# Performance work log

Measured on AMD Instinct MI355X. Metric: run time of the kernel, lower is better.

Reference implementation:

```python
import jax, jax.numpy as jnp
import numpy as np

H, W = 1080, 1920
NPART = 25          # BODY_25 joint parts (channel 25 is background)
NLIMB = 26          # 26 PAF limbs -> 52 PAF channels
K = 32              # max peaks kept per joint (static top-k)
MID = 10            # mid_num line samples
THRE1 = 0.1
SIGMA = 3.0
RADIUS = 12         # scipy gaussian_filter: int(truncate*sigma+0.5), truncate=4
# BODY_25 limb sequence (SKEL25DEF.paf_dict), paired with mapIdx [[2k,2k+1]]
LIMBS = np.array([[1,8],[1,2],[1,5],[2,3],[3,4],[5,6],[6,7],[8,9],[9,10],
                  [10,11],[8,12],[12,13],[13,14],[1,0],[0,15],[15,16],[0,17],
                  [0,18],[14,19],[19,20],[14,21],[11,22],[22,23],[11,24],
                  [2,17],[5,18]], dtype=np.int32)


def gaussian_blur(x):
    """Separable gaussian filter, sigma=3, scipy mode='reflect' (= np symmetric). x: [H,W,C]."""
    C = x.shape[-1]
    t = jnp.arange(-RADIUS, RADIUS + 1, dtype=x.dtype)
    k = jnp.exp(-0.5 * (t / SIGMA) ** 2)
    k = k / k.sum()
    dn = ('NHWC', 'HWIO', 'NHWC')
    # vertical pass
    xp = jnp.pad(x, ((RADIUS, RADIUS), (0, 0), (0, 0)), mode='symmetric')[None]
    kh = jnp.tile(k.reshape(-1, 1, 1, 1), (1, 1, 1, C))
    x1 = jax.lax.conv_general_dilated(xp, kh, (1, 1), 'VALID',
                                      dimension_numbers=dn, feature_group_count=C)
    # horizontal pass
    x1 = jnp.pad(x1, ((0, 0), (0, 0), (RADIUS, RADIUS), (0, 0)), mode='symmetric')
    kw = jnp.tile(k.reshape(1, -1, 1, 1), (1, 1, 1, C))
    x2 = jax.lax.conv_general_dilated(x1, kw, (1, 1), 'VALID',
                                      dimension_numbers=dn, feature_group_count=C)
    return x2[0]


def openpose_post(heatmap_avg, paf_avg):
    maps = heatmap_avg[:, :, :NPART]                      # [H,W,25] map_ori per part
    sm = gaussian_blur(maps)                              # one_heatmap per part
    z_row = jnp.zeros((1, W, NPART), sm.dtype)
    z_col = jnp.zeros((H, 1, NPART), sm.dtype)
    m_left = jnp.concatenate([z_row, sm[:-1]], axis=0)
    m_right = jnp.concatenate([sm[1:], z_row], axis=0)
    m_up = jnp.concatenate([z_col, sm[:, :-1]], axis=1)
    m_down = jnp.concatenate([sm[:, 1:], z_col], axis=1)
    peaks_bin = ((sm >= m_left) & (sm >= m_right) & (sm >= m_up)
                 & (sm >= m_down) & (sm > THRE1))
    # static per-part top-K peaks, scored by the ORIGINAL (unblurred) map value
    flat = jnp.where(peaks_bin, maps, -1e9).transpose(2, 0, 1).reshape(NPART, H * W)
    vals, idx = jax.lax.top_k(flat, K)                    # [25,K]
    mask = vals > -1e8
    py = (idx // W).astype(jnp.int32)
    px = (idx % W).astype(jnp.int32)
    peak_x = px.astype(maps.dtype)
    peak_y = py.astype(maps.dtype)
    peak_scores = jnp.where(mask, vals, 0.0)

    limbs = jnp.asarray(LIMBS)
    ax, ay, ma = peak_x[limbs[:, 0]], peak_y[limbs[:, 0]], mask[limbs[:, 0]]  # [26,K]
    bx, by, mb = peak_x[limbs[:, 1]], peak_y[limbs[:, 1]], mask[limbs[:, 1]]
    paf_pairs = jnp.moveaxis(paf_avg.reshape(H, W, NLIMB, 2), 2, 0)           # [26,H,W,2]

    def limb_conn(paf2, ax, ay, bx, by, ma, mb):
        vx = bx[None, :] - ax[:, None]                    # [K,K]
        vy = by[None, :] - ay[:, None]
        norm = jnp.sqrt(vx * vx + vy * vy) + 1e-10
        ux, uy = vx / norm, vy / norm
        t = jnp.linspace(0.0, 1.0, MID, dtype=ax.dtype)   # matches np.linspace(a,b,10)
        sx = jnp.round(ax[:, None, None] + vx[:, :, None] * t).astype(jnp.int32)  # [K,K,MID]
        sy = jnp.round(ay[:, None, None] + vy[:, :, None] * t).astype(jnp.int32)
        pvx = paf2[sy, sx, 0]
        pvy = paf2[sy, sx, 1]
        score = (pvx * ux[:, :, None] + pvy * uy[:, :, None]).mean(-1)
        score = jnp.clip(score, 0.0, 1.0)
        return jnp.where(ma[:, None] & mb[None, :], score, 0.0)

    conn = jax.vmap(limb_conn)(paf_pairs, ax, ay, bx, by, ma, mb)             # [26,K,K]
    return peak_x, peak_y, peak_scores, mask, conn


def setup_inputs() -> dict:
    key = jax.random.key(0)
    k1, k2 = jax.random.split(key)
    heatmap_avg = jax.random.uniform(k1, (H, W, NPART + 1), dtype=jnp.float32)
    paf_avg = jax.random.normal(k2, (H, W, 2 * NLIMB), dtype=jnp.float32) * 0.3
    return {"heatmap_avg": heatmap_avg, "paf_avg": paf_avg}


def reference(heatmap_avg, paf_avg):
    return openpose_post(heatmap_avg, paf_avg)
```

## Files before the change

kernel.cpp:

```cpp
#include <hip/hip_runtime.h>
#include <math.h>
#include <float.h>

#define H 1080
#define W 1920
#define HWSZ (H*W)
#define NPART 25
#define NCH 26
#define NLIMB 26
#define KTOP 32
#define MID 10
#define RAD 12

#define EPS1 4e-6f
#define EPS2 1.5e-7
#define BLCAP (1 << 20)
#define NS 16

#define VB 10
#define VXT 16
#define VCHUNK 100
#define TH2S 30
#define TW2B 256
#define VTC2 282
#define VTS2 283
#define SMS2 257
#define CANDC 2048

#define OFF_PY   800
#define OFF_SC   1600
#define OFF_MK   2400
#define OFF_CONN 3200

__device__ __constant__ int LIMBS_d[NLIMB * 2] = {
    1,8, 1,2, 1,5, 2,3, 3,4, 5,6, 6,7, 8,9, 9,10, 10,11, 8,12, 12,13, 13,14,
    1,0, 0,15, 15,16, 0,17, 0,18, 14,19, 19,20, 14,21, 11,22, 22,23, 11,24, 2,17, 5,18
};

__device__ __forceinline__ int symH(int y) {
    if (y < 0) return -1 - y;
    if (y >= H) return 2 * H - 1 - y;
    return y;
}
__device__ __forceinline__ int symW(int x) {
    if (x < 0) return -1 - x;
    if (x >= W) return 2 * W - 1 - x;
    return x;
}

__global__ void winit_k(double* __restrict__ gw64, float* __restrict__ gw32)
{
    if (threadIdx.x == 0) {
        double wd[25]; double s = 0.0;
        for (int t = 0; t < 25; ++t) {
            double u = (double)(t - 12) / 3.0;
            wd[t] = exp(-0.5 * u * u); s += wd[t];
        }
        for (int t = 0; t < 13; ++t) {
            double w = wd[t] / s;
            gw64[t] = w;
            gw32[t] = (float)w;
        }
    }
}

__global__ __launch_bounds__(416) void vert_k(
    const float* __restrict__ hm, float* __restrict__ vpl,
    const double* __restrict__ gw64)
{
    __shared__ float ldv[VB][26][17];
    const int tid = threadIdx.x;
    const int x0 = blockIdx.x * VXT;
    const int ys = blockIdx.y * VCHUNK;
    const int c  = tid % 26;
    const int xo = tid / 26;
    const int gx = x0 + xo;

    double ws[13];
    #pragma unroll
    for (int t = 0; t < 13; ++t) ws[t] = gw64[t];

    const size_t cstr = (size_t)W * NCH;
    const size_t base = (size_t)gx * NCH + c;
    const bool yint = (ys >= 12) && (ys + VCHUNK + 11 < H);

    double win[25];
    if (yint) {
        const float* p0 = hm + (size_t)(ys - 12) * cstr + base;
        #pragma unroll
        for (int k = 0; k < 24; ++k) { win[k] = (double)*p0; p0 += cstr; }
    } else {
        #pragma unroll
        for (int k = 0; k < 24; ++k) {
            int ry = symH(ys - 12 + k);
            win[k] = (double)hm[(size_t)ry * cstr + base];
        }
    }
    win[24] = 0.0;

    const float* pn = hm + (size_t)symH(ys + 12) * cstr + base;

    #pragma unroll 1
    for (int blk = 0; blk < VCHUNK; blk += 25) {
        #pragma unroll
        for (int p = 0; p < 25; ++p) {
            const int yo = blk + p;
            const int y  = ys + yo;
            double nv;
            if (yint) { nv = (double)*pn; pn += cstr; }
            else      { int ry = symH(y + 12); nv = (double)hm[(size_t)ry * cstr + base]; }
            win[(p + 24) % 25] = nv;
            double acc = 0.0;
            #pragma unroll
            for (int t = 0; t < 25; ++t)
                acc = fma(ws[t < 13 ? t : 24 - t], win[(p + t) % 25], acc);
            if (c < 25) ldv[yo % VB][c][xo] = (float)acc;
            if ((yo % VB) == VB - 1) {
                __syncthreads();
                const int c2 = tid >> 4, x2 = tid & 15;
                if (c2 < 25) {
                    const int yb = ys + yo - (VB - 1);
                    #pragma unroll
                    for (int i = 0; i < VB; ++i) {
                        int yr = yb + i;
                        if (yr < H)
                            vpl[(size_t)c2 * HWSZ + (size_t)yr * W + x0 + x2] = ldv[i][c2][x2];
                    }
                }
                __syncthreads();
            }
        }
    }
}

__global__ __launch_bounds__(512) void horiz_nms_k(
    const float* __restrict__ vpl, const float* __restrict__ hm,
    float* __restrict__ cval, int* __restrict__ cidx,
    int* __restrict__ counters, unsigned int* __restrict__ blg,
    const float* __restrict__ gw32, int cap)
{
    __shared__ __align__(16) float ubuf[32 * VTS2];
    float (*vt)[VTS2]  = reinterpret_cast<float(*)[VTS2]>(ubuf);
    float (*smt)[SMS2] = reinterpret_cast<float(*)[SMS2]>(ubuf);
    __shared__ unsigned short cand[CANDC];
    __shared__ unsigned int bl[1024];
    __shared__ int lcount, bcount, gbase, gbase2;

    const int tid = threadIdx.x;
    const int r   = tid & 31;
    const int g   = tid >> 5;
    const int ch  = blockIdx.z;
    const int x0  = blockIdx.x * TW2B;
    const int y0  = blockIdx.y * TH2S;
    const float* vp = vpl + (size_t)ch * HWSZ;

    if (tid == 0) { lcount = 0; bcount = 0; }
    float w32[13];
    #pragma unroll
    for (int t = 0; t < 13; ++t) w32[t] = gw32[t];

    {
        const int lr  = tid >> 4;
        const int lc0 = tid & 15;
        int gy = y0 - 1 + lr;
        gy = gy < 0 ? 0 : (gy >= H ? H - 1 : gy);
        const float* rowp = vp + (size_t)gy * W;
        const bool xint = (x0 >= 13) && (x0 + (VTC2 - 13) <= W);
        if (xint) {
            const float* p = rowp + (x0 - 13) + lc0;
            #pragma unroll
            for (int j = 0; j < 18; ++j) {
                int cc = lc0 + 16 * j;
                if (cc < VTC2) vt[lr][cc] = p[16 * j];
            }
        } else {
            #pragma unroll
            for (int j = 0; j < 18; ++j) {
                int cc = lc0 + 16 * j;
                if (cc < VTC2) vt[lr][cc] = rowp[symW(x0 - 13 + cc)];
            }
        }
    }
    __syncthreads();

    float a[18];
    #pragma unroll
    for (int k = 0; k < 18; ++k) a[k] = 0.f;
    {
        const float* vrow = &vt[r][g * 16];
        #pragma unroll
        for (int t = 0; t < 42; ++t) {
            float x = vrow[t];
            #pragma unroll
            for (int k = 0; k < 18; ++k)
                if (t >= k && t < k + 25) {
                    int wi = t - k; wi = wi < 13 ? wi : 24 - wi;
                    a[k] = fmaf(w32[wi], x, a[k]);
                }
        }
    }
    __syncthreads();

    const int gy_r = y0 - 1 + r;
    {
        const bool rowok = (gy_r >= 0 && gy_r < H);
        #pragma unroll
        for (int k = 1; k <= 16; ++k) {
            int j = g * 16 + k - 1;
            int gxj = x0 + j;
            smt[r][j] = (rowok && gxj < W) ? a[k] : 0.f;
        }
    }
    __syncthreads();

    if (r >= 1 && r <= TH2S && gy_r < H) {
        const float* up = &smt[r - 1][g * 16];
        const float* dn = &smt[r + 1][g * 16];
        const int ly = r - 1;
        #pragma unroll
        for (int k = 0; k < 16; ++k) {
            int gx = x0 + g * 16 + k;
            if (gx >= W) continue;
            float s  = a[k + 1];
            float lv = (gx == 0) ? 0.f : a[k];
            float rv = (gx + 1 >= W) ? 0.f : a[k + 2];
            float dT = s - 0.1f;
            float d0 = s - up[k];
            float d1 = s - dn[k];
            float d2 = s - lv;
            float d3 = s - rv;
            int flags = (fabsf(dT) <= EPS1 ? 1 : 0)
                      | (fabsf(d0) <= EPS1 ? 2 : 0)
                      | (fabsf(d1) <= EPS1 ? 4 : 0)
                      | (fabsf(d2) <= EPS1 ? 8 : 0)
                      | (fabsf(d3) <= EPS1 ? 16 : 0);
            if (!flags) {
                if (dT > 0.f && d0 >= 0.f && d1 >= 0.f && d2 >= 0.f && d3 >= 0.f) {
                    int pos = atomicAdd(&lcount, 1);
                    int gpix = (y0 + ly) * W + gx;
                    if (pos < CANDC) cand[pos] = (unsigned short)((ly << 8) | (g * 16 + k));
                    else {
                        int p = atomicAdd(&counters[ch], 1);
                        if (p < cap) {
                            cval[(size_t)ch * cap + p] = hm[(size_t)gpix * NCH + ch];
                            cidx[(size_t)ch * cap + p] = gpix;
                        }
                    }
                }
            } else {
                bool fail = (!(flags & 1)  && dT <= 0.f) ||
                            (!(flags & 2)  && d0 <  0.f) ||
                            (!(flags & 4)  && d1 <  0.f) ||
                            (!(flags & 8)  && d2 <  0.f) ||
                            (!(flags & 16) && d3 <  0.f);
                if (!fail) {
                    unsigned int ent = ((unsigned int)ch << 26) | ((unsigned int)flags << 21)
                                     | (unsigned int)((y0 + ly) * W + gx);
                    int bp = atomicAdd(&bcount, 1);
                    if (bp < 1024) bl[bp] = ent;
                    else {
                        int gp = atomicAdd(&counters[32], 1);
                        if (gp < BLCAP) blg[gp] = ent;
                    }
                }
            }
        }
    }
    __syncthreads();

    if (tid == 0) {
        int nl = lcount < CANDC ? lcount : CANDC;
        gbase  = atomicAdd(&counters[ch], nl);
        int nb = bcount < 1024 ? bcount : 1024;
        gbase2 = atomicAdd(&counters[32], nb);
    }
    __syncthreads();
    int n = lcount < CANDC ? lcount : CANDC;
    int b = gbase;
    for (int i = tid; i < n; i += 512) {
        int p = b + i;
        if (p < cap) {
            int e = cand[i];
            int ly = e >> 8, lx = e & 255;
            int gpix = (y0 + ly) * W + (x0 + lx);
            cval[(size_t)ch * cap + p] = hm[(size_t)gpix * NCH + ch];
            cidx[(size_t)ch * cap + p] = gpix;
        }
    }
    int nb = bcount < 1024 ? bcount : 1024;
    for (int i = tid; i < nb; i += 512) {
        int gp = gbase2 + i;
        if (gp < BLCAP) blg[gp] = bl[i];
    }
}

__device__ __forceinline__ double smh2(const float* __restrict__ vp,
                                       const double* w64s, int y, int x)
{
    int lane = threadIdx.x & 63;
    double term = 0.0;
    if (lane < 25) {
        int cx = symW(x - RAD + lane);
        int wi = lane < 13 ? lane : 24 - lane;
        term = w64s[wi] * (double)vp[(size_t)y * W + cx];
    }
    #pragma unroll
    for (int off = 16; off > 0; off >>= 1)
        term += __shfl_xor(term, off, 64);
    return __shfl(term, 0, 64);
}

__device__ double sm64_eval(const float* __restrict__ hm, int ch,
                            const double* w64s, int y, int x)
{
    int lane = threadIdx.x & 63;
    double colsum = 0.0;
    if (lane < 25) {
        int cx = symW(x - RAD + lane);
        float xv[25];
        #pragma unroll
        for (int t = 0; t < 25; t++) {
            int ry = symH(y - RAD + t);
            xv[t] = hm[((size_t)ry * W + cx) * NCH + ch];
        }
        #pragma unroll
        for (int t = 0; t < 25; t++)
            colsum = fma(w64s[t < 13 ? t : 24 - t], (double)xv[t], colsum);
    }
    double acc = 0.0;
    for (int ci = 0; ci < 25; ci++) {
        double cs = __shfl(colsum, ci, 64);
        acc = fma(w64s[ci < 13 ? ci : 24 - ci], cs, acc);
    }
    return acc;
}

__global__ __launch_bounds__(64) void recheck_k(
    const float* __restrict__ vpl, const float* __restrict__ hm,
    float* __restrict__ cval, int* __restrict__ cidx,
    int* __restrict__ counters, const unsigned int* __restrict__ blg,
    const double* __restrict__ gw64, int cap)
{
    __shared__ double w64s[13];
    const int tid = threadIdx.x;
    if (tid < 13) w64s[tid] = gw64[tid];
    __syncthreads();

    int total = counters[32];
    if (total > BLCAP) total = BLCAP;
    for (int e = blockIdx.x; e < total; e += gridDim.x) {
        unsigned int ent = blg[e];
        int ch    = (int)(ent >> 26);
        int flags = (int)((ent >> 21) & 31);
        int gpix  = (int)(ent & 0x1FFFFFu);
        int gy = gpix / W, gx = gpix - gy * W;
        const float* vp = vpl + (size_t)ch * HWSZ;

        double sc = smh2(vp, w64s, gy, gx);
        bool dead = false; bool esc = false;
        if (flags & 1) {
            double d = sc - 0.1;
            if (d <= -EPS2) dead = true; else if (d < EPS2) esc = true;
        }
        if (!dead && (flags & 2)) {
            double nv = (gy - 1 >= 0) ? smh2(vp, w64s, gy - 1, gx) : 0.0;
            double d = sc - nv;
            if (d <= -EPS2) dead = true; else if (d < EPS2) esc = true;
        }
        if (!dead && (flags & 4)) {
            double nv = (gy + 1 < H) ? smh2(vp, w64s, gy + 1, gx) : 0.0;
            double d = sc - nv;
            if (d <= -EPS2) dead = true; else if (d < EPS2) esc = true;
        }
        if (!dead && (flags & 8)) {
            double nv = (gx - 1 >= 0) ? smh2(vp, w64s, gy, gx - 1) : 0.0;
            double d = sc - nv;
            if (d <= -EPS2) dead = true; else if (d < EPS2) esc = true;
        }
        if (!dead && (flags & 16)) {
            double nv = (gx + 1 < W) ? smh2(vp, w64s, gy, gx + 1) : 0.0;
            double d = sc - nv;
            if (d <= -EPS2) dead = true; else if (d < EPS2) esc = true;
        }
        bool accept = false;
        if (!dead && !esc) accept = true;
        else if (!dead && esc) {
            double sE = sm64_eval(hm, ch, w64s, gy, gx);
            bool ok = (flags & 1) ? (sE > 0.1) : true;
            if (ok && (flags & 2))  { double nv = (gy - 1 >= 0) ? sm64_eval(hm, ch, w64s, gy - 1, gx) : 0.0; ok = (sE >= nv); }
            if (ok && (flags & 4))  { double nv = (gy + 1 <  H) ? sm64_eval(hm, ch, w64s, gy + 1, gx) : 0.0; ok = (sE >= nv); }
            if (ok && (flags & 8))  { double nv = (gx - 1 >= 0) ? sm64_eval(hm, ch, w64s, gy, gx - 1) : 0.0; ok = (sE >= nv); }
            if (ok && (flags & 16)) { double nv = (gx + 1 <  W) ? sm64_eval(hm, ch, w64s, gy, gx + 1) : 0.0; ok = (sE >= nv); }
            accept = ok;
        }
        if (accept && tid == 0) {
            int p = atomicAdd(&counters[ch], 1);
            if (p < cap) {
                cval[(size_t)ch * cap + p] = hm[(size_t)gpix * NCH + ch];
                cidx[(size_t)ch * cap + p] = gpix;
            }
        }
    }
}

#define TH 32
#define TW 64
#define LR (TH + 2*RAD + 2)
#define LC 90
#define VRR 34
#define VC (TW + 2*RAD + 2)
#define SR 34
#define SC 66
__global__ __launch_bounds__(256) void blur_peaks_gather(
    const float* __restrict__ hm,
    float* __restrict__ cval, int* __restrict__ cidx,
    int* __restrict__ counters, int cap)
{
    __shared__ float  in_t[LR][LC];
    __shared__ double v[VRR][VC];
    __shared__ double smv[SR][SC];
    __shared__ double wgt[2 * RAD + 1];
    __shared__ double wsum;

    const int tid = threadIdx.x;
    const int ch  = blockIdx.x;
    const int x0  = blockIdx.y * TW;
    const int y0  = blockIdx.z * TH;

    if (tid < 2 * RAD + 1) {
        double t = (double)(tid - RAD) / 3.0;
        wgt[tid] = exp(-0.5 * t * t);
    }
    __syncthreads();
    if (tid == 0) {
        double s = 0.0;
        for (int i = 0; i < 2 * RAD + 1; i++) s += wgt[i];
        wsum = s;
    }
    __syncthreads();
    if (tid < 2 * RAD + 1) wgt[tid] /= wsum;

    for (int i = tid; i < LR * LC; i += 256) {
        int r = i / LC, c = i % LC;
        int gy = symH(y0 - RAD - 1 + r);
        int gx = symW(x0 - RAD - 1 + c);
        in_t[r][c] = hm[((size_t)gy * W + gx) * NCH + ch];
    }
    __syncthreads();

    for (int i = tid; i < VRR * VC; i += 256) {
        int r = i / VC, c = i % VC;
        double acc = 0.0;
        #pragma unroll
        for (int t = 0; t < 2 * RAD + 1; t++)
            acc = fma(wgt[t], (double)in_t[r + t][c], acc);
        v[r][c] = acc;
    }
    __syncthreads();

    for (int i = tid; i < SR * SC; i += 256) {
        int r = i / SC, cc = i % SC;
        int gy = y0 - 1 + r;
        int gx = x0 - 1 + cc;
        double acc = 0.0;
        if (gy >= 0 && gy < H && gx >= 0 && gx < W) {
            #pragma unroll
            for (int t = 0; t < 2 * RAD + 1; t++)
                acc = fma(wgt[t], v[r][cc + t], acc);
        }
        smv[r][cc] = acc;
    }
    __syncthreads();

    for (int i = tid; i < TH * TW; i += 256) {
        int ly = i / TW, lx = i % TW;
        int gy = y0 + ly, gx = x0 + lx;
        if (gy >= H || gx >= W) continue;
        double s = smv[ly + 1][lx + 1];
        if (s > 0.1 &&
            s >= smv[ly][lx + 1] && s >= smv[ly + 2][lx + 1] &&
            s >= smv[ly + 1][lx] && s >= smv[ly + 1][lx + 2]) {
            float val = in_t[ly + RAD + 1][lx + RAD + 1];
            int pos = atomicAdd(&counters[ch], 1);
            if (pos < cap) {
                cval[(size_t)ch * cap + pos] = val;
                cidx[(size_t)ch * cap + pos] = gy * W + gx;
            }
        }
    }
}

#define BT 128
__global__ __launch_bounds__(BT) void topk1_kernel(
    const float* __restrict__ cval, const int* __restrict__ cidx,
    const int* __restrict__ counters, int cap,
    unsigned long long* __restrict__ s1)
{
    __shared__ unsigned long long lk[KTOP * BT];
    __shared__ unsigned long long rk[BT];
    __shared__ int rw[BT];
    __shared__ int winner;

    const int tid = threadIdx.x;
    const int sl  = blockIdx.x;
    const int ch  = blockIdx.y;
    int n = counters[ch];
    if (n > cap) n = cap;

    int cnt = 0;
    for (int j = sl * BT + tid; j < n; j += NS * BT) {
        float v = cval[(size_t)ch * cap + j];
        unsigned int u = __float_as_uint(v);
        u = (u & 0x80000000u) ? ~u : (u | 0x80000000u);
        unsigned long long key =
            ((unsigned long long)u << 32) |
            (unsigned int)(0xFFFFFFFFu - (unsigned int)cidx[(size_t)ch * cap + j]);
        if (cnt == KTOP) {
            if (key <= lk[(KTOP - 1) * BT + tid]) continue;
            cnt = KTOP - 1;
        }
        int i = cnt;
        while (i > 0 && key > lk[(i - 1) * BT + tid]) {
            lk[i * BT + tid] = lk[(i - 1) * BT + tid];
            i--;
        }
        lk[i * BT + tid] = key;
        cnt++;
    }
    int cur = 0;
    __syncthreads();

    for (int k = 0; k < KTOP; k++) {
        rk[tid] = (cur < cnt) ? lk[cur * BT + tid] : 0ULL;
        rw[tid] = tid;
        __syncthreads();
        for (int s = BT / 2; s > 0; s >>= 1) {
            if (tid < s) {
                if (rk[tid + s] > rk[tid]) { rk[tid] = rk[tid + s]; rw[tid] = rw[tid + s]; }
            }
            __syncthreads();
        }
        if (tid == 0) {
            winner = rw[0];
            s1[((size_t)ch * NS + sl) * KTOP + k] = rk[0];
        }
        __syncthreads();
        if (tid == winner && cur < cnt) cur++;
        __syncthreads();
    }
}

__global__ __launch_bounds__(BT) void topk2_kernel(
    const unsigned long long* __restrict__ s1,
    const int* __restrict__ counters, int cap, float* __restrict__ out)
{
    __shared__ unsigned long long sk[NS * KTOP];
    const int tid = threadIdx.x;
    const int ch  = blockIdx.x;

    for (int i = tid; i < NS * KTOP; i += BT)
        sk[i] = s1[(size_t)ch * NS * KTOP + i];
    __syncthreads();

    for (int k = 2; k <= NS * KTOP; k <<= 1) {
        for (int j = k >> 1; j > 0; j >>= 1) {
            for (int t = tid; t < NS * KTOP; t += BT) {
                int ixj = t ^ j;
                if (ixj > t) {
                    unsigned long long a = sk[t], b = sk[ixj];
                    bool sw = ((t & k) == 0) ? (a < b) : (a > b);
                    if (sw) { sk[t] = b; sk[ixj] = a; }
                }
            }
            __syncthreads();
        }
    }

    int n = counters[ch];
    if (n > cap) n = cap;
    if (tid < KTOP) {
        unsigned long long bk = sk[tid];
        float px, py, sc, mk;
        if (bk == 0ULL) {
            int fake = tid - n; if (fake < 0) fake = 0;
            px = (float)(fake % W); py = (float)(fake / W); sc = 0.f; mk = 0.f;
        } else {
            unsigned int u = (unsigned int)(bk >> 32);
            unsigned int fb = (u & 0x80000000u) ? (u ^ 0x80000000u) : ~u;
            float v = __uint_as_float(fb);
            int idx = (int)(0xFFFFFFFFu - (unsigned int)(bk & 0xFFFFFFFFu));
            px = (float)(idx % W); py = (float)(idx / W); sc = v; mk = 1.f;
        }
        out[ch * KTOP + tid]          = px;
        out[OFF_PY + ch * KTOP + tid] = py;
        out[OFF_SC + ch * KTOP + tid] = sc;
        out[OFF_MK + ch * KTOP + tid] = mk;
    }
}

__global__ __launch_bounds__(BT) void topk_kernel(
    const float* __restrict__ cval, const int* __restrict__ cidx,
    const int* __restrict__ counters, int cap, float* __restrict__ out)
{
    __shared__ unsigned long long lk[KTOP * BT];
    __shared__ unsigned long long rk[BT];
    __shared__ int rw[BT];
    __shared__ int winner;

    const int tid = threadIdx.x;
    const int ch  = blockIdx.x;
    int n = counters[ch];
    if (n > cap) n = cap;

    int cnt = 0;
    for (int j = tid; j < n; j += BT) {
        float v = cval[(size_t)ch * cap + j];
        unsigned int u = __float_as_uint(v);
        u = (u & 0x80000000u) ? ~u : (u | 0x80000000u);
        unsigned long long key =
            ((unsigned long long)u << 32) |
            (unsigned int)(0xFFFFFFFFu - (unsigned int)cidx[(size_t)ch * cap + j]);
        if (cnt == KTOP) {
            if (key <= lk[(KTOP - 1) * BT + tid]) continue;
            cnt = KTOP - 1;
        }
        int i = cnt;
        while (i > 0 && key > lk[(i - 1) * BT + tid]) {
            lk[i * BT + tid] = lk[(i - 1) * BT + tid];
            i--;
        }
        lk[i * BT + tid] = key;
        cnt++;
    }
    int cur = 0;
    __syncthreads();

    for (int k = 0; k < KTOP; k++) {
        rk[tid] = (cur < cnt) ? lk[cur * BT + tid] : 0ULL;
        rw[tid] = tid;
        __syncthreads();
        for (int s = BT / 2; s > 0; s >>= 1) {
            if (tid < s) {
                if (rk[tid + s] > rk[tid]) { rk[tid] = rk[tid + s]; rw[tid] = rw[tid + s]; }
            }
            __syncthreads();
        }
        if (tid == 0) {
            winner = rw[0];
            unsigned long long bk = rk[0];
            float px, py, sc, mk;
            if (bk == 0ULL) {
                int fake = k - n; if (fake < 0) fake = 0;
                px = (float)(fake % W); py = (float)(fake / W); sc = 0.f; mk = 0.f;
            } else {
                unsigned int u = (unsigned int)(bk >> 32);
                unsigned int fb = (u & 0x80000000u) ? (u ^ 0x80000000u) : ~u;
                float v = __uint_as_float(fb);
                int idx = (int)(0xFFFFFFFFu - (unsigned int)(bk & 0xFFFFFFFFu));
                px = (float)(idx % W); py = (float)(idx / W); sc = v; mk = 1.f;
            }
            out[ch * KTOP + k]          = px;
            out[OFF_PY + ch * KTOP + k] = py;
            out[OFF_SC + ch * KTOP + k] = sc;
            out[OFF_MK + ch * KTOP + k] = mk;
        }
        __syncthreads();
        if (tid == winner && cur < cnt) cur++;
        __syncthreads();
    }
}

__global__ __launch_bounds__(1024) void limbs_kernel(
    const float* __restrict__ pk, const float* __restrict__ paf,
    float* __restrict__ out)
{
    const int l = blockIdx.x;
    const int tid = threadIdx.x;
    const int i = tid >> 5;
    const int j = tid & 31;
    const int A = LIMBS_d[2 * l], B = LIMBS_d[2 * l + 1];

    float ax = pk[A * KTOP + i],          ay = pk[OFF_PY + A * KTOP + i];
    float ma = pk[OFF_MK + A * KTOP + i];
    float bx = pk[B * KTOP + j],          by = pk[OFF_PY + B * KTOP + j];
    float mb = pk[OFF_MK + B * KTOP + j];

    float vx = bx - ax, vy = by - ay;
    float norm = sqrtf(vx * vx + vy * vy) + 1e-10f;
    float ux = vx / norm, uy = vy / norm;

    const float step = 1.0f / 9.0f;
    float sum = 0.f;
    #pragma unroll
    for (int m = 0; m < MID; m++) {
        float t = (float)m * step;
        int sx = (int)rintf(ax + vx * t);
        int sy = (int)rintf(ay + vy * t);
        const float* p = paf + ((size_t)sy * W + sx) * (2 * NLIMB) + 2 * l;
        sum += p[0] * ux + p[1] * uy;
    }
    float score = sum / (float)MID;
    score = score < 0.f ? 0.f : (score > 1.f ? 1.f : score);
    float res = (ma != 0.f && mb != 0.f) ? score : 0.f;
    out[OFF_CONN + l * (KTOP * KTOP) + i * KTOP + j] = res;
}

extern "C" void kernel_launch(void* const* d_in, const int* in_sizes, int n_in,
                              void* d_out, int out_size, void* d_ws, size_t ws_size,
                              hipStream_t stream)
{
    const float* hm  = (const float*)d_in[0];
    const float* paf = (const float*)d_in[1];
    float* out = (float*)d_out;

    const size_t vpl_bytes = (size_t)NPART * HWSZ * sizeof(float);
    const size_t bl_bytes  = (size_t)BLCAP * 4;
    const size_t s1_bytes  = (size_t)NPART * NS * KTOP * 8;
    const size_t head = 512;

    bool pathA = false;
    int cap = 1;
    if (ws_size > head + vpl_bytes + bl_bytes + s1_bytes
                 + (size_t)NPART * 8 * 4096 + 1024) {
        size_t avail = ws_size - head - vpl_bytes - bl_bytes - s1_bytes - 1024;
        long long c = (long long)(avail / ((size_t)NPART * 8));
        cap = c > 65536 ? 65536 : (int)c;
        pathA = true;
    } else {
        size_t avail = ws_size > head ? ws_size - head : 0;
        long long c = (long long)(avail / ((size_t)NPART * 8));
        cap = c > 65536 ? 65536 : (int)c;
        if (cap < 1) cap = 1;
    }

    int*    counters = (int*)d_ws;
    double* gw64 = (double*)((char*)d_ws + 256);
    float*  gw32 = (float*)((char*)d_ws + 384);
    float* cval = (float*)((char*)d_ws + head);
    int*   cidx = (int*)(cval + (size_t)NPART * cap);
    unsigned long long* s1 = (unsigned long long*)(cidx + (size_t)NPART * cap);
    unsigned int* blg = (unsigned int*)(s1 + (pathA ? (size_t)NPART * NS * KTOP : 0));
    float* vpl = (float*)(blg + (pathA ? (size_t)BLCAP : 0));
    vpl = (float*)(((uintptr_t)vpl + 255) & ~(uintptr_t)255);

    hipMemsetAsync(d_ws, 0, 256, stream);

    if (pathA) {
        winit_k<<<1, 64, 0, stream>>>(gw64, gw32);
        dim3 g1(W / VXT, (H + VCHUNK - 1) / VCHUNK);
        vert_k<<<g1, 416, 0, stream>>>(hm, vpl, gw64);
        dim3 g2((W + TW2B - 1) / TW2B, H / TH2S, NPART);
        horiz_nms_k<<<g2, 512, 0, stream>>>(vpl, hm, cval, cidx, counters, blg, gw32, cap);
        recheck_k<<<2048, 64, 0, stream>>>(vpl, hm, cval, cidx, counters, blg, gw64, cap);
        dim3 gt(NS, NPART);
        topk1_kernel<<<gt, BT, 0, stream>>>(cval, cidx, counters, cap, s1);
        topk2_kernel<<<NPART, BT, 0, stream>>>(s1, counters, cap, out);
    } else {
        dim3 gA(NPART, (W + TW - 1) / TW, (H + TH - 1) / TH);
        blur_peaks_gather<<<gA, 256, 0, stream>>>(hm, cval, cidx, counters, cap);
        topk_kernel<<<NPART, BT, 0, stream>>>(cval, cidx, counters, cap, out);
    }
    limbs_kernel<<<NLIMB, 1024, 0, stream>>>(out, paf, out);
}
```

Before: 442.3 us.

## Fuse double-precision borderline recheck into horizontal NMS kernel using LDS tile

Borderline peak candidates are now rechecked in double precision inside horiz_nms_k, reading the vertical-pass tile already held in shared memory. This replaces the global borderline list and the separate wave-per-entry recheck kernel that re-read vpl. Only the rare ambiguous cases are escalated to a smaller exact-evaluation kernel. Up/down neighbour values now come from wave shuffles instead of a second shared-memory pass with two barriers, and vert_k skips loads for the idle 26th channel lane. The cost is more divergent double-precision work inside the NMS kernel and a smaller global escalation buffer capacity.

```diff
diff --git a/kernel.cpp b/kernel.cpp
--- a/kernel.cpp
+++ b/kernel.cpp
@@ -14,7 +14,7 @@
 
 #define EPS1 4e-6f
 #define EPS2 1.5e-7
-#define BLCAP (1 << 20)
+#define B3CAP 65536
 #define NS 16
 
 #define VB 10
@@ -24,8 +24,7 @@
 #define TW2B 256
 #define VTC2 282
 #define VTS2 283
-#define SMS2 257
-#define CANDC 2048
+#define CANDC 1024
 
 #define OFF_PY   800
 #define OFF_SC   1600
@@ -75,6 +74,7 @@
     const int c  = tid % 26;
     const int xo = tid / 26;
     const int gx = x0 + xo;
+    const bool act = (c < 25);
 
     double ws[13];
     #pragma unroll
@@ -85,18 +85,21 @@
     const bool yint = (ys >= 12) && (ys + VCHUNK + 11 < H);
 
     double win[25];
-    if (yint) {
-        const float* p0 = hm + (size_t)(ys - 12) * cstr + base;
-        #pragma unroll
-        for (int k = 0; k < 24; ++k) { win[k] = (double)*p0; p0 += cstr; }
-    } else {
-        #pragma unroll
-        for (int k = 0; k < 24; ++k) {
-            int ry = symH(ys - 12 + k);
-            win[k] = (double)hm[(size_t)ry * cstr + base];
-        }
-    }
-    win[24] = 0.0;
+    #pragma unroll
+    for (int k = 0; k < 25; ++k) win[k] = 0.0;
+    if (act) {
+        if (yint) {
+            const float* p0 = hm + (size_t)(ys - 12) * cstr + base;
+            #pragma unroll
+            for (int k = 0; k < 24; ++k) { win[k] = (double)*p0; p0 += cstr; }
+        } else {
+            #pragma unroll
+            for (int k = 0; k < 24; ++k) {
+                int ry = symH(ys - 12 + k);
+                win[k] = (double)hm[(size_t)ry * cstr + base];
+            }
+        }
+    }
 
     const float* pn = hm + (size_t)symH(ys + 12) * cstr + base;
 
@@ -106,15 +109,15 @@
         for (int p = 0; p < 25; ++p) {
             const int yo = blk + p;
             const int y  = ys + yo;
-            double nv;
-            if (yint) { nv = (double)*pn; pn += cstr; }
-            else      { int ry = symH(y + 12); nv = (double)hm[(size_t)ry * cstr + base]; }
+            double nv = 0.0;
+            if (yint) { if (act) nv = (double)*pn; pn += cstr; }
+            else if (act) { int ry = symH(y + 12); nv = (double)hm[(size_t)ry * cstr + base]; }
             win[(p + 24) % 25] = nv;
             double acc = 0.0;
             #pragma unroll
             for (int t = 0; t < 25; ++t)
                 acc = fma(ws[t < 13 ? t : 24 - t], win[(p + t) % 25], acc);
-            if (c < 25) ldv[yo % VB][c][xo] = (float)acc;
+            if (act) ldv[yo % VB][c][xo] = (float)acc;
             if ((yo % VB) == VB - 1) {
                 __syncthreads();
                 const int c2 = tid >> 4, x2 = tid & 15;
@@ -133,18 +136,28 @@
     }
 }
 
+__device__ __forceinline__ double smh2_lds(const float (*vt)[VTS2],
+                                           const double* __restrict__ gw64,
+                                           int row, int cb)
+{
+    double acc = 0.0;
+    #pragma unroll
+    for (int t = 0; t < 25; ++t) {
+        int wi = t < 13 ? t : 24 - t;
+        acc = fma(gw64[wi], (double)vt[row][cb + t], acc);
+    }
+    return acc;
+}
+
 __global__ __launch_bounds__(512) void horiz_nms_k(
     const float* __restrict__ vpl, const float* __restrict__ hm,
     float* __restrict__ cval, int* __restrict__ cidx,
-    int* __restrict__ counters, unsigned int* __restrict__ blg,
-    const float* __restrict__ gw32, int cap)
-{
-    __shared__ __align__(16) float ubuf[32 * VTS2];
-    float (*vt)[VTS2]  = reinterpret_cast<float(*)[VTS2]>(ubuf);
-    float (*smt)[SMS2] = reinterpret_cast<float(*)[SMS2]>(ubuf);
+    int* __restrict__ counters, unsigned int* __restrict__ bl3,
+    const float* __restrict__ gw32, const double* __restrict__ gw64, int cap)
+{
+    __shared__ __align__(16) float vt[32][VTS2];
     __shared__ unsigned short cand[CANDC];
-    __shared__ unsigned int bl[1024];
-    __shared__ int lcount, bcount, gbase, gbase2;
+    __shared__ int lcount, gbase;
 
     const int tid = threadIdx.x;
     const int r   = tid & 31;
@@ -154,7 +167,7 @@
     const int y0  = blockIdx.y * TH2S;
     const float* vp = vpl + (size_t)ch * HWSZ;
 
-    if (tid == 0) { lcount = 0; bcount = 0; }
+    if (tid == 0) lcount = 0;
     float w32[13];
     #pragma unroll
     for (int t = 0; t < 13; ++t) w32[t] = gw32[t];
@@ -199,23 +212,16 @@
                 }
         }
     }
-    __syncthreads();
-
-    const int gy_r = y0 - 1 + r;
-    {
-        const bool rowok = (gy_r >= 0 && gy_r < H);
-        #pragma unroll
-        for (int k = 1; k <= 16; ++k) {
-            int j = g * 16 + k - 1;
-            int gxj = x0 + j;
-            smt[r][j] = (rowok && gxj < W) ? a[k] : 0.f;
-        }
-    }
-    __syncthreads();
-
-    if (r >= 1 && r <= TH2S && gy_r < H) {
-        const float* up = &smt[r - 1][g * 16];
-        const float* dn = &smt[r + 1][g * 16];
+
+    float upv[16], dnv[16];
+    #pragma unroll
+    for (int k = 0; k < 16; ++k) {
+        upv[k] = __shfl_up(a[k + 1], 1, 64);
+        dnv[k] = __shfl_down(a[k + 1], 1, 64);
+    }
+
+    const int gy = y0 - 1 + r;
+    if (r >= 1 && r <= TH2S && gy < H) {
         const int ly = r - 1;
         #pragma unroll
         for (int k = 0; k < 16; ++k) {
@@ -224,9 +230,11 @@
             float s  = a[k + 1];
             float lv = (gx == 0) ? 0.f : a[k];
             float rv = (gx + 1 >= W) ? 0.f : a[k + 2];
+            float u0 = (gy - 1 >= 0) ? upv[k] : 0.f;
+            float d0v = (gy + 1 < H) ? dnv[k] : 0.f;
             float dT = s - 0.1f;
-            float d0 = s - up[k];
-            float d1 = s - dn[k];
+            float d0 = s - u0;
+            float d1 = s - d0v;
             float d2 = s - lv;
             float d3 = s - rv;
             int flags = (fabsf(dT) <= EPS1 ? 1 : 0)
@@ -234,19 +242,10 @@
                       | (fabsf(d1) <= EPS1 ? 4 : 0)
                       | (fabsf(d2) <= EPS1 ? 8 : 0)
                       | (fabsf(d3) <= EPS1 ? 16 : 0);
+            bool emit = false;
+            bool esc  = false;
             if (!flags) {
-                if (dT > 0.f && d0 >= 0.f && d1 >= 0.f && d2 >= 0.f && d3 >= 0.f) {
-                    int pos = atomicAdd(&lcount, 1);
-                    int gpix = (y0 + ly) * W + gx;
-                    if (pos < CANDC) cand[pos] = (unsigned short)((ly << 8) | (g * 16 + k));
-                    else {
-                        int p = atomicAdd(&counters[ch], 1);
-                        if (p < cap) {
-                            cval[(size_t)ch * cap + p] = hm[(size_t)gpix * NCH + ch];
-                            cidx[(size_t)ch * cap + p] = gpix;
-                        }
-                    }
-                }
+                emit = (dT > 0.f && d0 >= 0.f && d1 >= 0.f && d2 >= 0.f && d3 >= 0.f);
             } else {
                 bool fail = (!(flags & 1)  && dT <= 0.f) ||
                             (!(flags & 2)  && d0 <  0.f) ||
@@ -254,25 +253,63 @@
                             (!(flags & 8)  && d2 <  0.f) ||
                             (!(flags & 16) && d3 <  0.f);
                 if (!fail) {
-                    unsigned int ent = ((unsigned int)ch << 26) | ((unsigned int)flags << 21)
-                                     | (unsigned int)((y0 + ly) * W + gx);
-                    int bp = atomicAdd(&bcount, 1);
-                    if (bp < 1024) bl[bp] = ent;
-                    else {
-                        int gp = atomicAdd(&counters[32], 1);
-                        if (gp < BLCAP) blg[gp] = ent;
+                    const int cb = g * 16 + k + 1;
+                    double s2 = smh2_lds(vt, gw64, r, cb);
+                    bool dead = false;
+                    if (flags & 1) {
+                        double d = s2 - 0.1;
+                        if (d <= -EPS2) dead = true; else if (d < EPS2) esc = true;
+                    }
+                    if (!dead && (flags & 2)) {
+                        double nv = (gy - 1 >= 0) ? smh2_lds(vt, gw64, r - 1, cb) : 0.0;
+                        double d = s2 - nv;
+                        if (d <= -EPS2) dead = true; else if (d < EPS2) esc = true;
+                    }
+                    if (!dead && (flags & 4)) {
+                        double nv = (gy + 1 < H) ? smh2_lds(vt, gw64, r + 1, cb) : 0.0;
+                        double d = s2 - nv;
+                        if (d <= -EPS2) dead = true; else if (d < EPS2) esc = true;
+                    }
+                    if (!dead && (flags & 8)) {
+                        double nv = (gx - 1 >= 0) ? smh2_lds(vt, gw64, r, cb - 1) : 0.0;
+                        double d = s2 - nv;
+                        if (d <= -EPS2) dead = true; else if (d < EPS2) esc = true;
+                    }
+                    if (!dead && (flags & 16)) {
+                        double nv = (gx + 1 < W) ? smh2_lds(vt, gw64, r, cb + 1) : 0.0;
+                        double d = s2 - nv;
+                        if (d <= -EPS2) dead = true; else if (d < EPS2) esc = true;
+                    }
+                    if (!dead) {
+                        if (esc) {
+                            unsigned int ent = ((unsigned int)ch << 26)
+                                             | ((unsigned int)flags << 21)
+                                             | (unsigned int)(gy * W + gx);
+                            int gp = atomicAdd(&counters[33], 1);
+                            if (gp < B3CAP) bl3[gp] = ent;
+                        } else emit = true;
                     }
                 }
             }
+            if (emit) {
+                int pos = atomicAdd(&lcount, 1);
+                if (pos < CANDC) cand[pos] = (unsigned short)((ly << 8) | (g * 16 + k));
+                else {
+                    int gpix = gy * W + gx;
+                    int p = atomicAdd(&counters[ch], 1);
+                    if (p < cap) {
+                        cval[(size_t)ch * cap + p] = hm[(size_t)gpix * NCH + ch];
+                        cidx[(size_t)ch * cap + p] = gpix;
+                    }
+                }
+            }
         }
     }
     __syncthreads();
 
     if (tid == 0) {
         int nl = lcount < CANDC ? lcount : CANDC;
-        gbase  = atomicAdd(&counters[ch], nl);
-        int nb = bcount < 1024 ? bcount : 1024;
-        gbase2 = atomicAdd(&counters[32], nb);
+        gbase = atomicAdd(&counters[ch], nl);
     }
     __syncthreads();
     int n = lcount < CANDC ? lcount : CANDC;
@@ -287,27 +324,6 @@
             cidx[(size_t)ch * cap + p] = gpix;
         }
     }
-    int nb = bcount < 1024 ? bcount : 1024;
-    for (int i = tid; i < nb; i += 512) {
-        int gp = gbase2 + i;
-        if (gp < BLCAP) blg[gp] = bl[i];
-    }
-}
-
-__device__ __forceinline__ double smh2(const float* __restrict__ vp,
-                                       const double* w64s, int y, int x)
-{
-    int lane = threadIdx.x & 63;
-    double term = 0.0;
-    if (lane < 25) {
-        int cx = symW(x - RAD + lane);
-        int wi = lane < 13 ? lane : 24 - lane;
-        term = w64s[wi] * (double)vp[(size_t)y * W + cx];
-    }
-    #pragma unroll
-    for (int off = 16; off > 0; off >>= 1)
-        term += __shfl_xor(term, off, 64);
-    return __shfl(term, 0, 64);
 }
 
 __device__ double sm64_eval(const float* __restrict__ hm, int ch,
@@ -335,10 +351,10 @@
     return acc;
 }
 
-__global__ __launch_bounds__(64) void recheck_k(
-    const float* __restrict__ vpl, const float* __restrict__ hm,
+__global__ __launch_bounds__(64) void recheck3_k(
+    const float* __restrict__ hm,
     float* __restrict__ cval, int* __restrict__ cidx,
-    int* __restrict__ counters, const unsigned int* __restrict__ blg,
+    int* __restrict__ counters, const unsigned int* __restrict__ bl3,
     const double* __restrict__ gw64, int cap)
 {
     __shared__ double w64s[13];
@@ -346,54 +362,21 @@
     if (tid < 13) w64s[tid] = gw64[tid];
     __syncthreads();
 
-    int total = counters[32];
-    if (total > BLCAP) total = BLCAP;
+    int total = counters[33];
+    if (total > B3CAP) total = B3CAP;
     for (int e = blockIdx.x; e < total; e += gridDim.x) {
-        unsigned int ent = blg[e];
+        unsigned int ent = bl3[e];
         int ch    = (int)(ent >> 26);
         int flags = (int)((ent >> 21) & 31);
         int gpix  = (int)(ent & 0x1FFFFFu);
         int gy = gpix / W, gx = gpix - gy * W;
-        const float* vp = vpl + (size_t)ch * HWSZ;
-
-        double sc = smh2(vp, w64s, gy, gx);
-        bool dead = false; bool esc = false;
-        if (flags & 1) {
-            double d = sc - 0.1;
-            if (d <= -EPS2) dead = true; else if (d < EPS2) esc = true;
-        }
-        if (!dead && (flags & 2)) {
-            double nv = (gy - 1 >= 0) ? smh2(vp, w64s, gy - 1, gx) : 0.0;
-            double d = sc - nv;
-            if (d <= -EPS2) dead = true; else if (d < EPS2) esc = true;
-        }
-        if (!dead && (flags & 4)) {
-            double nv = (gy + 1 < H) ? smh2(vp, w64s, gy + 1, gx) : 0.0;
-            double d = sc - nv;
-            if (d <= -EPS2) dead = true; else if (d < EPS2) esc = true;
-        }
-        if (!dead && (flags & 8)) {
-            double nv = (gx - 1 >= 0) ? smh2(vp, w64s, gy, gx - 1) : 0.0;
-            double d = sc - nv;
-            if (d <= -EPS2) dead = true; else if (d < EPS2) esc = true;
-        }
-        if (!dead && (flags & 16)) {
-            double nv = (gx + 1 < W) ? smh2(vp, w64s, gy, gx + 1) : 0.0;
-            double d = sc - nv;
-            if (d <= -EPS2) dead = true; else if (d < EPS2) esc = true;
-        }
-        bool accept = false;
-        if (!dead && !esc) accept = true;
-        else if (!dead && esc) {
-            double sE = sm64_eval(hm, ch, w64s, gy, gx);
-            bool ok = (flags & 1) ? (sE > 0.1) : true;
-            if (ok && (flags & 2))  { double nv = (gy - 1 >= 0) ? sm64_eval(hm, ch, w64s, gy - 1, gx) : 0.0; ok = (sE >= nv); }
-            if (ok && (flags & 4))  { double nv = (gy + 1 <  H) ? sm64_eval(hm, ch, w64s, gy + 1, gx) : 0.0; ok = (sE >= nv); }
-            if (ok && (flags & 8))  { double nv = (gx - 1 >= 0) ? sm64_eval(hm, ch, w64s, gy, gx - 1) : 0.0; ok = (sE >= nv); }
-            if (ok && (flags & 16)) { double nv = (gx + 1 <  W) ? sm64_eval(hm, ch, w64s, gy, gx + 1) : 0.0; ok = (sE >= nv); }
-            accept = ok;
-        }
-        if (accept && tid == 0) {
+        double sc = sm64_eval(hm, ch, w64s, gy, gx);
+        bool ok = (flags & 1) ? (sc > 0.1) : true;
+        if (ok && (flags & 2))  { double nv = (gy - 1 >= 0) ? sm64_eval(hm, ch, w64s, gy - 1, gx) : 0.0; ok = (sc >= nv); }
+        if (ok && (flags & 4))  { double nv = (gy + 1 <  H) ? sm64_eval(hm, ch, w64s, gy + 1, gx) : 0.0; ok = (sc >= nv); }
+        if (ok && (flags & 8))  { double nv = (gx - 1 >= 0) ? sm64_eval(hm, ch, w64s, gy, gx - 1) : 0.0; ok = (sc >= nv); }
+        if (ok && (flags & 16)) { double nv = (gx + 1 <  W) ? sm64_eval(hm, ch, w64s, gy, gx + 1) : 0.0; ok = (sc >= nv); }
+        if (tid == 0 && ok) {
             int p = atomicAdd(&counters[ch], 1);
             if (p < cap) {
                 cval[(size_t)ch * cap + p] = hm[(size_t)gpix * NCH + ch];
@@ -714,15 +697,15 @@
     float* out = (float*)d_out;
 
     const size_t vpl_bytes = (size_t)NPART * HWSZ * sizeof(float);
-    const size_t bl_bytes  = (size_t)BLCAP * 4;
+    const size_t b3_bytes  = (size_t)B3CAP * 4;
     const size_t s1_bytes  = (size_t)NPART * NS * KTOP * 8;
     const size_t head = 512;
 
     bool pathA = false;
     int cap = 1;
-    if (ws_size > head + vpl_bytes + bl_bytes + s1_bytes
+    if (ws_size > head + vpl_bytes + b3_bytes + s1_bytes
                  + (size_t)NPART * 8 * 4096 + 1024) {
-        size_t avail = ws_size - head - vpl_bytes - bl_bytes - s1_bytes - 1024;
+        size_t avail = ws_size - head - vpl_bytes - b3_bytes - s1_bytes - 1024;
         long long c = (long long)(avail / ((size_t)NPART * 8));
         cap = c > 65536 ? 65536 : (int)c;
         pathA = true;
@@ -739,8 +722,8 @@
     float* cval = (float*)((char*)d_ws + head);
     int*   cidx = (int*)(cval + (size_t)NPART * cap);
     unsigned long long* s1 = (unsigned long long*)(cidx + (size_t)NPART * cap);
-    unsigned int* blg = (unsigned int*)(s1 + (pathA ? (size_t)NPART * NS * KTOP : 0));
-    float* vpl = (float*)(blg + (pathA ? (size_t)BLCAP : 0));
+    unsigned int* bl3 = (unsigned int*)(s1 + (pathA ? (size_t)NPART * NS * KTOP : 0));
+    float* vpl = (float*)(bl3 + (pathA ? (size_t)B3CAP : 0));
     vpl = (float*)(((uintptr_t)vpl + 255) & ~(uintptr_t)255);
 
     hipMemsetAsync(d_ws, 0, 256, stream);
@@ -750,8 +733,8 @@
         dim3 g1(W / VXT, (H + VCHUNK - 1) / VCHUNK);
         vert_k<<<g1, 416, 0, stream>>>(hm, vpl, gw64);
         dim3 g2((W + TW2B - 1) / TW2B, H / TH2S, NPART);
-        horiz_nms_k<<<g2, 512, 0, stream>>>(vpl, hm, cval, cidx, counters, blg, gw32, cap);
-        recheck_k<<<2048, 64, 0, stream>>>(vpl, hm, cval, cidx, counters, blg, gw64, cap);
+        horiz_nms_k<<<g2, 512, 0, stream>>>(vpl, hm, cval, cidx, counters, bl3, gw32, gw64, cap);
+        recheck3_k<<<128, 64, 0, stream>>>(hm, cval, cidx, counters, bl3, gw64, cap);
         dim3 gt(NS, NPART);
         topk1_kernel<<<gt, BT, 0, stream>>>(cval, cidx, counters, cap, s1);
         topk2_kernel<<<NPART, BT, 0, stream>>>(s1, counters, cap, out);
```

After: 532.8 us. 1.2x slower.
